# Kernel tuning notes

Measured on AMD Instinct MI355X. Metric: run time of the kernel, lower is better.

## Reference

```python
import jax, jax.numpy as jnp
import numpy as np

K_HOPS = 10
ALPHA = 0.1
N_NODES = 50000
N_EDGES = 600000
F_IN = 128
HIDDEN = 64
N_CLASSES = 40


def setup_inputs() -> dict:
    key = jax.random.key(0)
    k1, k2, k3, k4 = jax.random.split(key, 4)
    x = jax.random.normal(k1, (N_NODES, F_IN), dtype=jnp.float32)
    edge_index = jax.random.randint(k2, (2, N_EDGES), 0, N_NODES, dtype=jnp.int32)
    edge_weight = jnp.ones((N_EDGES,), dtype=jnp.float32)
    W1 = jax.random.normal(k3, (F_IN, HIDDEN), dtype=jnp.float32) * (1.0 / np.sqrt(F_IN))
    b1 = jnp.zeros((HIDDEN,), dtype=jnp.float32)
    W2 = jax.random.normal(k4, (HIDDEN, N_CLASSES), dtype=jnp.float32) * (1.0 / np.sqrt(HIDDEN))
    b2 = jnp.zeros((N_CLASSES,), dtype=jnp.float32)
    return {"x": x, "edge_index": edge_index, "edge_weight": edge_weight,
            "W1": W1, "b1": b1, "W2": W2, "b2": b2}


def reference(x, edge_index, edge_weight, W1, b1, W2, b2):
    n = x.shape[0]
    # GCN symmetric normalization with self-loops (tfg gcn cache)
    self_idx = jnp.arange(n, dtype=edge_index.dtype)
    row = jnp.concatenate([edge_index[0], self_idx])
    col = jnp.concatenate([edge_index[1], self_idx])
    w = jnp.concatenate([edge_weight, jnp.ones((n,), dtype=edge_weight.dtype)])
    deg = jax.ops.segment_sum(w, row, num_segments=n)
    dinv = jnp.where(deg > 0, jax.lax.rsqrt(jnp.maximum(deg, 1e-12)), 0.0)
    nw = dinv[row] * w * dinv[col]  # [E+N] normalized edge weights

    def prop(h):
        # h_out[i] = sum_{(i,j)} nw * h[j]
        return jax.ops.segment_sum(h[col] * nw[:, None], row, num_segments=n)

    def step(h, _):
        h_next = prop(h)
        return h_next, None

    # SSGC: out = (1-alpha)/K * sum_{l=1..K} T^l x + alpha * x
    def step_acc(carry, _):
        h, acc = carry
        h_next = prop(h)
        return (h_next, acc + h_next), None

    (_, acc), _ = jax.lax.scan(step_acc, (x, jnp.zeros_like(x)), None, length=K_HOPS)
    h = (1.0 - ALPHA) / K_HOPS * acc + ALPHA * x  # [N, F]

    h = jax.nn.relu(h @ W1 + b1)  # [N, HIDDEN]
    logits = h @ W2 + b2          # [N, N_CLASSES]
    return logits
```

## Files before the change

kernel.cpp:

```cpp
#include <hip/hip_runtime.h>
#include <hip/hip_fp16.h>
#include <math.h>

constexpr int   N   = 50000;
constexpr int   E   = 600000;
constexpr int   FIN = 128;
constexpr int   H   = 64;
constexpr int   C   = 40;
constexpr int   K   = 10;
constexpr float CK  = (1.0f - 0.1f) / 10.0f;
constexpr float AL  = 0.1f;

typedef float v2f __attribute__((ext_vector_type(2)));

__device__ __forceinline__ unsigned pack_fp8x4(float f0, float f1, float f2, float f3) {
    unsigned r = __builtin_amdgcn_cvt_pk_fp8_f32(f0, f1, 0u, false);
    r = __builtin_amdgcn_cvt_pk_fp8_f32(f2, f3, r, true);
    return r;
}

__device__ __forceinline__ float ep_w(unsigned v) {
    return __half2float(__ushort_as_half((unsigned short)(v >> 16)));
}
__device__ __forceinline__ unsigned ep_pack(int c, float w) {
    return (unsigned)(unsigned short)c |
           ((unsigned)__half_as_ushort(__float2half_rn(w)) << 16);
}

__device__ __forceinline__ void accum4(float* s, unsigned v, float w) {
    v2f p0 = __builtin_amdgcn_cvt_pk_f32_fp8(v, false);
    v2f p1 = __builtin_amdgcn_cvt_pk_f32_fp8(v, true);
    s[0] = fmaf(w, p0.x, s[0]); s[1] = fmaf(w, p0.y, s[1]);
    s[2] = fmaf(w, p1.x, s[2]); s[3] = fmaf(w, p1.y, s[3]);
}

constexpr int G1N  = 64;
constexpr int XPAD = 132;
__global__ __launch_bounds__(256, 2) void k_gemm1(const float* __restrict__ x,
                                                  const float* __restrict__ W1,
                                                  float* __restrict__ y0,
                                                  unsigned char* __restrict__ y0f8) {
    __shared__ float ws[FIN * H];
    __shared__ float xs[G1N * XPAD];
    const float4* W14 = (const float4*)W1;
    const float4* x4  = (const float4*)x;
    int t = threadIdx.x;
    int node0 = blockIdx.x * G1N;
    for (int i = t; i < FIN * H / 4; i += 256) ((float4*)ws)[i] = W14[i];
    for (int p = 0; p < 8; ++p) {
        int idx = p * 256 + t;
        int n   = idx >> 5;
        int kk  = idx & 31;
        int node = node0 + n;
        float4 v = (node < N) ? x4[(size_t)node * (FIN / 4) + kk]
                              : make_float4(0.f, 0.f, 0.f, 0.f);
        *(float4*)(xs + n * XPAD + kk * 4) = v;
    }
    __syncthreads();
    int nb = (t >> 4) * 4;
    int cb = (t & 15) * 4;
    float a00=0,a01=0,a02=0,a03=0, a10=0,a11=0,a12=0,a13=0;
    float a20=0,a21=0,a22=0,a23=0, a30=0,a31=0,a32=0,a33=0;
#pragma unroll 8
    for (int k = 0; k < FIN; ++k) {
        float4 wv = *(const float4*)(ws + k * H + cb);
        float x0 = xs[(nb + 0) * XPAD + k];
        float x1 = xs[(nb + 1) * XPAD + k];
        float x2 = xs[(nb + 2) * XPAD + k];
        float x3 = xs[(nb + 3) * XPAD + k];
        a00 = fmaf(x0, wv.x, a00); a01 = fmaf(x0, wv.y, a01);
        a02 = fmaf(x0, wv.z, a02); a03 = fmaf(x0, wv.w, a03);
        a10 = fmaf(x1, wv.x, a10); a11 = fmaf(x1, wv.y, a11);
        a12 = fmaf(x1, wv.z, a12); a13 = fmaf(x1, wv.w, a13);
        a20 = fmaf(x2, wv.x, a20); a21 = fmaf(x2, wv.y, a21);
        a22 = fmaf(x2, wv.z, a22); a23 = fmaf(x2, wv.w, a23);
        a30 = fmaf(x3, wv.x, a30); a31 = fmaf(x3, wv.y, a31);
        a32 = fmaf(x3, wv.z, a32); a33 = fmaf(x3, wv.w, a33);
    }
    float4 rows[4] = {make_float4(a00,a01,a02,a03), make_float4(a10,a11,a12,a13),
                      make_float4(a20,a21,a22,a23), make_float4(a30,a31,a32,a33)};
#pragma unroll
    for (int i = 0; i < 4; ++i) {
        int node = node0 + nb + i;
        if (node >= N) break;
        float4 r = rows[i];
        *(float4*)(y0 + (size_t)node * H + cb) = r;
        *(unsigned*)(y0f8 + (size_t)node * H + cb) = pack_fp8x4(r.x, r.y, r.z, r.w);
    }
}

__global__ __launch_bounds__(256) void k_count(const int* __restrict__ row,
                                               int* __restrict__ cnt8,
                                               unsigned short* __restrict__ rank) {
    int base = blockIdx.x * 1024 + threadIdx.x;
    int copy = blockIdx.x & 7;
#pragma unroll
    for (int i = 0; i < 4; ++i) {
        int e = base + i * 256;
        if (e < E) {
            int r = row[e];
            int old = atomicAdd(&cnt8[(size_t)copy * N + r], 1);
            rank[e] = (unsigned short)old;
        }
    }
}

__global__ __launch_bounds__(1024) void k_scan_blocks(const int* __restrict__ cnt8,
                                                      int* __restrict__ row_ptr,
                                                      int* __restrict__ bsum) {
    __shared__ int s[1024];
    int gid = blockIdx.x * 1024 + threadIdx.x;
    int v = 0;
    if (gid < N) {
#pragma unroll
        for (int c = 0; c < 8; ++c) v += cnt8[(size_t)c * N + gid];
        v = (v + 3) & ~3;
    }
    s[threadIdx.x] = v;
    __syncthreads();
    for (int off = 1; off < 1024; off <<= 1) {
        int t = (threadIdx.x >= off) ? s[threadIdx.x - off] : 0;
        __syncthreads();
        s[threadIdx.x] += t;
        __syncthreads();
    }
    if (gid < N) row_ptr[gid] = s[threadIdx.x] - v;
    if (threadIdx.x == 1023) bsum[blockIdx.x] = s[1023];
}

__global__ void k_scan_sums(const int* __restrict__ bsum, int* __restrict__ boff, int nb,
                            int* __restrict__ rowN) {
    int lane = threadIdx.x;
    int orig = (lane < nb) ? bsum[lane] : 0;
    int v = orig;
    for (int off = 1; off < 64; off <<= 1) {
        int t = __shfl_up(v, off, 64);
        if (lane >= off) v += t;
    }
    if (lane < nb) boff[lane] = v - orig;
    if (lane == nb - 1) *rowN = v;
}

__global__ __launch_bounds__(1024) void k_addoff(int* __restrict__ row_ptr,
                                                 const int* __restrict__ boff,
                                                 int* __restrict__ cnt8,
                                                 unsigned* __restrict__ ep) {
    int gid = blockIdx.x * 1024 + threadIdx.x;
    if (gid < N) {
        int rp = row_ptr[gid] + boff[blockIdx.x];
        row_ptr[gid] = rp;
        int off = rp;
        int real = 0;
#pragma unroll
        for (int c = 0; c < 8; ++c) {
            int t = cnt8[(size_t)c * N + gid];
            cnt8[(size_t)c * N + gid] = off;
            off += t;
            real += t;
        }
        int pd = (real + 3) & ~3;
        for (int j = real; j < pd; ++j) ep[rp + j] = 0u;
    }
    if (gid == 0) {
        int tot = row_ptr[N];
        *(uint4*)(ep + tot) = make_uint4(0u, 0u, 0u, 0u);
    }
}

__global__ __launch_bounds__(256) void k_scatter(const int* __restrict__ row,
                                                 const int* __restrict__ col,
                                                 const float* __restrict__ w,
                                                 const unsigned short* __restrict__ rank,
                                                 const int* __restrict__ base8,
                                                 unsigned* __restrict__ ep) {
    int base = blockIdx.x * 1024 + threadIdx.x;
    int copy = blockIdx.x & 7;
#pragma unroll
    for (int i = 0; i < 4; ++i) {
        int e = base + i * 256;
        if (e < E) {
            int r = row[e];
            int p = base8[(size_t)copy * N + r] + rank[e];
            ep[p] = ep_pack(col[e], w[e]);
        }
    }
}

__global__ void k_deg_dinv(const unsigned* __restrict__ ep, const int* __restrict__ row_ptr,
                           float* __restrict__ dinv, float* __restrict__ dinv2) {
    int i = blockIdx.x * blockDim.x + threadIdx.x;
    if (i >= N) return;
    float d = 1.0f;
    int e0 = row_ptr[i], e1 = row_ptr[i + 1];
    for (int j = e0; j < e1; ++j) d += ep_w(ep[j]);
    float di = rsqrtf(d);
    dinv[i]  = di;
    dinv2[i] = di * di;
}

__global__ __launch_bounds__(256) void k_norm(unsigned* __restrict__ ep,
                                              const int* __restrict__ row_ptr,
                                              const float* __restrict__ dinv) {
    int node = blockIdx.x * 32 + (threadIdx.x >> 3);
    if (node >= N) return;
    int l = threadIdx.x & 7;
    float dr = dinv[node];
    int e0 = row_ptr[node], e1 = row_ptr[node + 1];
    for (int j = e0 + l; j < e1; j += 8) {
        unsigned v = ep[j];
        int c = v & 0xFFFFu;
        ep[j] = ep_pack(c, ep_w(v) * dr * dinv[c]);
    }
}

constexpr int HSP = 68;
template <bool WRITE_H, bool ACC_INIT, bool FINAL>
__global__ __launch_bounds__(256) void k_prop(const unsigned* __restrict__ hin,
                                              unsigned* __restrict__ hout,
                                              __half* __restrict__ acch,
                                              const float* __restrict__ dinv2,
                                              const int* __restrict__ row_ptr,
                                              const unsigned* __restrict__ ep,
                                              const float4* __restrict__ y04,
                                              const float* __restrict__ b1,
                                              const float* __restrict__ W2,
                                              const float* __restrict__ b2,
                                              float* __restrict__ out) {
    extern __shared__ float smem[];
    float* w2s = smem;
    float* hs  = smem + H * C;
    float* b2s = hs + 16 * HSP;
    float* b1s = b2s + C;
    int t = threadIdx.x;
    if (FINAL) {
        for (int i = t; i < H * C; i += 256) w2s[i] = W2[i];
        if (t < C) b2s[t] = b2[t];
        if (t < H) b1s[t] = b1[t];
        __syncthreads();
    }
    int lane = t & 63;
    int nib  = (t >> 6) * 4 + (lane >> 4);
    int l    = lane & 15;
    int node = blockIdx.x * 16 + nib;
    bool nv  = node < N;
    int nodec = nv ? node : N - 1;
    int start = row_ptr[nodec];
    int pdeg  = nv ? (row_ptr[nodec + 1] - start) : 0;
    int md = pdeg;
#pragma unroll
    for (int off = 16; off <= 32; off <<= 1) md = max(md, __shfl_xor(md, off, 64));

    size_t base = (size_t)nodec * 16 + l;
    unsigned vself = hin[base];
    float d2       = dinv2[nodec];
    uint2* ap = (uint2*)(acch + (size_t)nodec * H + l * 4);
    uint2 old;
    if (nv && (FINAL || !ACC_INIT)) old = *ap;

    float s[4];
#pragma unroll
    for (int i = 0; i < 4; ++i) s[i] = 0.f;

    const unsigned* rp = ep + start;
    uint4 ea = *(const uint4*)rp;
    uint4 eb = *(const uint4*)(rp + ((4 < pdeg) ? 4 : 0));
    for (int batch = 0; batch < md; batch += 8) {
        uint4 ca = ea, cb = eb;
        int n0 = batch + 8, n1 = batch + 12;
        ea = *(const uint4*)(rp + ((n0 < pdeg) ? n0 : 0));
        eb = *(const uint4*)(rp + ((n1 < pdeg) ? n1 : 0));
        unsigned v0 = hin[(size_t)(ca.x & 0xFFFFu) * 16 + l];
        unsigned v1 = hin[(size_t)(ca.y & 0xFFFFu) * 16 + l];
        unsigned v2 = hin[(size_t)(ca.z & 0xFFFFu) * 16 + l];
        unsigned v3 = hin[(size_t)(ca.w & 0xFFFFu) * 16 + l];
        unsigned v4 = hin[(size_t)(cb.x & 0xFFFFu) * 16 + l];
        unsigned v5 = hin[(size_t)(cb.y & 0xFFFFu) * 16 + l];
        unsigned v6 = hin[(size_t)(cb.z & 0xFFFFu) * 16 + l];
        unsigned v7 = hin[(size_t)(cb.w & 0xFFFFu) * 16 + l];
        accum4(s, v0, (batch     < pdeg) ? ep_w(ca.x) : 0.0f);
        accum4(s, v1, (batch + 1 < pdeg) ? ep_w(ca.y) : 0.0f);
        accum4(s, v2, (batch + 2 < pdeg) ? ep_w(ca.z) : 0.0f);
        accum4(s, v3, (batch + 3 < pdeg) ? ep_w(ca.w) : 0.0f);
        accum4(s, v4, (batch + 4 < pdeg) ? ep_w(cb.x) : 0.0f);
        accum4(s, v5, (batch + 5 < pdeg) ? ep_w(cb.y) : 0.0f);
        accum4(s, v6, (batch + 6 < pdeg) ? ep_w(cb.z) : 0.0f);
        accum4(s, v7, (batch + 7 < pdeg) ? ep_w(cb.w) : 0.0f);
    }
    if (nv) {
        accum4(s, vself, d2);
        if (WRITE_H) {
            hout[base] = pack_fp8x4(s[0], s[1], s[2], s[3]);
        }
        if (FINAL) {
            const unsigned* u = (const unsigned*)&old;
#pragma unroll
            for (int d = 0; d < 2; ++d) {
                float2 f = __half22float2(*(__half2*)&u[d]);
                s[2*d+0] += f.x; s[2*d+1] += f.y;
            }
            float4 ya = y04[(size_t)nodec * (H / 4) + l];
            const float* bp = b1s + l * 4;
            float* hp = hs + nib * HSP + l * 4;
            hp[0] = fmaxf(fmaf(CK, s[0], fmaf(AL, ya.x, bp[0])), 0.f);
            hp[1] = fmaxf(fmaf(CK, s[1], fmaf(AL, ya.y, bp[1])), 0.f);
            hp[2] = fmaxf(fmaf(CK, s[2], fmaf(AL, ya.z, bp[2])), 0.f);
            hp[3] = fmaxf(fmaf(CK, s[3], fmaf(AL, ya.w, bp[3])), 0.f);
        } else {
            if (!ACC_INIT) {
                const unsigned* u = (const unsigned*)&old;
#pragma unroll
                for (int d = 0; d < 2; ++d) {
                    float2 f = __half22float2(*(__half2*)&u[d]);
                    s[2*d+0] += f.x; s[2*d+1] += f.y;
                }
            }
            uint2 nvp;
            unsigned* u = (unsigned*)&nvp;
#pragma unroll
            for (int d = 0; d < 2; ++d) {
                __half2 h = __floats2half2_rn(s[2*d+0], s[2*d+1]);
                u[d] = *(unsigned*)&h;
            }
            *ap = nvp;
        }
    }
    if (FINAL) {
        __syncthreads();
        int node0 = blockIdx.x * 16;
        for (int o = t; o < 16 * C; o += 256) {
            int nl = o / C, c = o % C;
            int n2 = node0 + nl;
            if (n2 >= N) continue;
            float v = b2s[c];
            const float* hr = &hs[nl * HSP];
#pragma unroll
            for (int k = 0; k < H; ++k) v = fmaf(hr[k], w2s[k * C + c], v);
            out[n2 * C + c] = v;
        }
    }
}

extern "C" void kernel_launch(void* const* d_in, const int* in_sizes, int n_in,
                              void* d_out, int out_size, void* d_ws, size_t ws_size,
                              hipStream_t stream) {
    const float* x  = (const float*)d_in[0];
    const int*   ei = (const int*)d_in[1];
    const float* ew = (const float*)d_in[2];
    const float* W1 = (const float*)d_in[3];
    const float* b1 = (const float*)d_in[4];
    const float* W2 = (const float*)d_in[5];
    const float* b2 = (const float*)d_in[6];
    float* out = (float*)d_out;

    const int* row = ei;
    const int* col = ei + E;

    char* ws = (char*)d_ws;
    size_t off = 0;
    auto alloc = [&](size_t bytes) -> char* {
        char* p = ws + off;
        off = (off + bytes + 1023) & ~(size_t)1023;
        return p;
    };
    constexpr size_t EPAD = (size_t)E + 3 * (size_t)N + 1024;
    float*          y0   = (float*)alloc((size_t)N * H * 4);
    unsigned char*  y0f8 = (unsigned char*)alloc((size_t)N * H);
    unsigned char*  ha   = (unsigned char*)alloc((size_t)N * H);
    unsigned char*  hb   = (unsigned char*)alloc((size_t)N * H);
    __half*         acch = (__half*)alloc((size_t)N * H * 2);
    int*            cnt8 = (int*)alloc((size_t)8 * N * 4);
    unsigned short* rank = (unsigned short*)alloc((size_t)E * 2);
    float*    dinv   = (float*)   alloc((size_t)N * 4);
    float*    dinv2  = (float*)   alloc((size_t)N * 4);
    int*      row_ptr= (int*)     alloc((size_t)(N + 1) * 4);
    int*      bsum   = (int*)     alloc(64 * 4);
    int*      boff   = (int*)     alloc(64 * 4);
    unsigned* ep     = (unsigned*)alloc(EPAD * 4);

    hipMemsetAsync(cnt8, 0, (size_t)8 * N * 4, stream);

    k_gemm1<<<(N + G1N - 1) / G1N, 256, 0, stream>>>(x, W1, y0, y0f8);

    k_count<<<(E + 1023) / 1024, 256, 0, stream>>>(row, cnt8, rank);

    constexpr int NB = (N + 1023) / 1024;
    k_scan_blocks<<<NB, 1024, 0, stream>>>(cnt8, row_ptr, bsum);
    k_scan_sums<<<1, 64, 0, stream>>>(bsum, boff, NB, row_ptr + N);
    k_addoff<<<NB, 1024, 0, stream>>>(row_ptr, boff, cnt8, ep);

    k_scatter<<<(E + 1023) / 1024, 256, 0, stream>>>(row, col, ew, rank, cnt8, ep);
    k_deg_dinv<<<(N + 255) / 256, 256, 0, stream>>>(ep, row_ptr, dinv, dinv2);
    k_norm<<<(N + 31) / 32, 256, 0, stream>>>(ep, row_ptr, dinv);

    const unsigned* hin = (const unsigned*)y0f8;
    unsigned* bufs[2] = {(unsigned*)ha, (unsigned*)hb};
    const float4* y04 = (const float4*)y0;
    int grid = (N + 15) / 16;
    size_t smemF = (size_t)(H * C + 16 * HSP + C + H) * 4;
    for (int hop = 0; hop < K; ++hop) {
        unsigned* hout = bufs[hop & 1];
        if (hop == 0)
            k_prop<true, true, false><<<grid, 256, 0, stream>>>(hin, hout, acch, dinv2,
                row_ptr, ep, y04, b1, W2, b2, out);
        else if (hop == K - 1)
            k_prop<false, false, true><<<grid, 256, smemF, stream>>>(hin, hout, acch, dinv2,
                row_ptr, ep, y04, b1, W2, b2, out);
        else
            k_prop<true, false, false><<<grid, 256, 0, stream>>>(hin, hout, acch, dinv2,
                row_ptr, ep, y04, b1, W2, b2, out);
        hin = hout;
    }
}
```

Baseline: 293.1 us.

## Deepen gather prefetch in propagation and spread count kernel over more blocks

The propagation loop now software-pipelines two stages ahead: edge records are prefetched 16 entries ahead and the feature gathers for the next batch are issued before the current batch is accumulated, so more memory loads are in flight per thread. The accumulator read is moved after the neighbour loop to shorten register live ranges. The count kernel now processes one edge per thread with four times more blocks, and the scatter kernel derives the counter copy from the edge index so the two kernels stay consistent. This costs more registers in the hot kernel, which may lower occupancy.

```diff
diff --git a/kernel.cpp b/kernel.cpp
--- a/kernel.cpp
+++ b/kernel.cpp
@@ -92,17 +92,12 @@
 __global__ __launch_bounds__(256) void k_count(const int* __restrict__ row,
                                                int* __restrict__ cnt8,
                                                unsigned short* __restrict__ rank) {
-    int base = blockIdx.x * 1024 + threadIdx.x;
+    int e = blockIdx.x * 256 + threadIdx.x;
+    if (e >= E) return;
     int copy = blockIdx.x & 7;
-#pragma unroll
-    for (int i = 0; i < 4; ++i) {
-        int e = base + i * 256;
-        if (e < E) {
-            int r = row[e];
-            int old = atomicAdd(&cnt8[(size_t)copy * N + r], 1);
-            rank[e] = (unsigned short)old;
-        }
-    }
+    int r = row[e];
+    int old = atomicAdd(&cnt8[(size_t)copy * N + r], 1);
+    rank[e] = (unsigned short)old;
 }
 
 __global__ __launch_bounds__(1024) void k_scan_blocks(const int* __restrict__ cnt8,
@@ -174,11 +169,11 @@
                                                  const int* __restrict__ base8,
                                                  unsigned* __restrict__ ep) {
     int base = blockIdx.x * 1024 + threadIdx.x;
-    int copy = blockIdx.x & 7;
 #pragma unroll
     for (int i = 0; i < 4; ++i) {
         int e = base + i * 256;
         if (e < E) {
+            int copy = (e >> 8) & 7;
             int r = row[e];
             int p = base8[(size_t)copy * N + r] + rank[e];
             ep[p] = ep_pack(col[e], w[e]);
@@ -253,45 +248,58 @@
     size_t base = (size_t)nodec * 16 + l;
     unsigned vself = hin[base];
     float d2       = dinv2[nodec];
-    uint2* ap = (uint2*)(acch + (size_t)nodec * H + l * 4);
-    uint2 old;
-    if (nv && (FINAL || !ACC_INIT)) old = *ap;
 
     float s[4];
 #pragma unroll
     for (int i = 0; i < 4; ++i) s[i] = 0.f;
 
     const unsigned* rp = ep + start;
-    uint4 ea = *(const uint4*)rp;
-    uint4 eb = *(const uint4*)(rp + ((4 < pdeg) ? 4 : 0));
-    for (int batch = 0; batch < md; batch += 8) {
-        uint4 ca = ea, cb = eb;
-        int n0 = batch + 8, n1 = batch + 12;
-        ea = *(const uint4*)(rp + ((n0 < pdeg) ? n0 : 0));
-        eb = *(const uint4*)(rp + ((n1 < pdeg) ? n1 : 0));
-        unsigned v0 = hin[(size_t)(ca.x & 0xFFFFu) * 16 + l];
-        unsigned v1 = hin[(size_t)(ca.y & 0xFFFFu) * 16 + l];
-        unsigned v2 = hin[(size_t)(ca.z & 0xFFFFu) * 16 + l];
-        unsigned v3 = hin[(size_t)(ca.w & 0xFFFFu) * 16 + l];
-        unsigned v4 = hin[(size_t)(cb.x & 0xFFFFu) * 16 + l];
-        unsigned v5 = hin[(size_t)(cb.y & 0xFFFFu) * 16 + l];
-        unsigned v6 = hin[(size_t)(cb.z & 0xFFFFu) * 16 + l];
-        unsigned v7 = hin[(size_t)(cb.w & 0xFFFFu) * 16 + l];
-        accum4(s, v0, (batch     < pdeg) ? ep_w(ca.x) : 0.0f);
-        accum4(s, v1, (batch + 1 < pdeg) ? ep_w(ca.y) : 0.0f);
-        accum4(s, v2, (batch + 2 < pdeg) ? ep_w(ca.z) : 0.0f);
-        accum4(s, v3, (batch + 3 < pdeg) ? ep_w(ca.w) : 0.0f);
-        accum4(s, v4, (batch + 4 < pdeg) ? ep_w(cb.x) : 0.0f);
-        accum4(s, v5, (batch + 5 < pdeg) ? ep_w(cb.y) : 0.0f);
-        accum4(s, v6, (batch + 6 < pdeg) ? ep_w(cb.z) : 0.0f);
-        accum4(s, v7, (batch + 7 < pdeg) ? ep_w(cb.w) : 0.0f);
+    if (md > 0) {
+        uint4 rA0 = *(const uint4*)rp;
+        uint4 rA1 = *(const uint4*)(rp + ((4  < pdeg) ? 4  : 0));
+        uint4 rB0 = *(const uint4*)(rp + ((8  < pdeg) ? 8  : 0));
+        uint4 rB1 = *(const uint4*)(rp + ((12 < pdeg) ? 12 : 0));
+        unsigned g0 = hin[(size_t)(rA0.x & 0xFFFFu) * 16 + l];
+        unsigned g1 = hin[(size_t)(rA0.y & 0xFFFFu) * 16 + l];
+        unsigned g2 = hin[(size_t)(rA0.z & 0xFFFFu) * 16 + l];
+        unsigned g3 = hin[(size_t)(rA0.w & 0xFFFFu) * 16 + l];
+        unsigned g4 = hin[(size_t)(rA1.x & 0xFFFFu) * 16 + l];
+        unsigned g5 = hin[(size_t)(rA1.y & 0xFFFFu) * 16 + l];
+        unsigned g6 = hin[(size_t)(rA1.z & 0xFFFFu) * 16 + l];
+        unsigned g7 = hin[(size_t)(rA1.w & 0xFFFFu) * 16 + l];
+        for (int b = 0; b < md; b += 8) {
+            int n0 = b + 16, n1 = b + 20;
+            uint4 rC0 = *(const uint4*)(rp + ((n0 < pdeg) ? n0 : 0));
+            uint4 rC1 = *(const uint4*)(rp + ((n1 < pdeg) ? n1 : 0));
+            unsigned h0 = hin[(size_t)(rB0.x & 0xFFFFu) * 16 + l];
+            unsigned h1 = hin[(size_t)(rB0.y & 0xFFFFu) * 16 + l];
+            unsigned h2 = hin[(size_t)(rB0.z & 0xFFFFu) * 16 + l];
+            unsigned h3 = hin[(size_t)(rB0.w & 0xFFFFu) * 16 + l];
+            unsigned h4 = hin[(size_t)(rB1.x & 0xFFFFu) * 16 + l];
+            unsigned h5 = hin[(size_t)(rB1.y & 0xFFFFu) * 16 + l];
+            unsigned h6 = hin[(size_t)(rB1.z & 0xFFFFu) * 16 + l];
+            unsigned h7 = hin[(size_t)(rB1.w & 0xFFFFu) * 16 + l];
+            accum4(s, g0, (b     < pdeg) ? ep_w(rA0.x) : 0.0f);
+            accum4(s, g1, (b + 1 < pdeg) ? ep_w(rA0.y) : 0.0f);
+            accum4(s, g2, (b + 2 < pdeg) ? ep_w(rA0.z) : 0.0f);
+            accum4(s, g3, (b + 3 < pdeg) ? ep_w(rA0.w) : 0.0f);
+            accum4(s, g4, (b + 4 < pdeg) ? ep_w(rA1.x) : 0.0f);
+            accum4(s, g5, (b + 5 < pdeg) ? ep_w(rA1.y) : 0.0f);
+            accum4(s, g6, (b + 6 < pdeg) ? ep_w(rA1.z) : 0.0f);
+            accum4(s, g7, (b + 7 < pdeg) ? ep_w(rA1.w) : 0.0f);
+            rA0 = rB0; rA1 = rB1; rB0 = rC0; rB1 = rC1;
+            g0 = h0; g1 = h1; g2 = h2; g3 = h3;
+            g4 = h4; g5 = h5; g6 = h6; g7 = h7;
+        }
     }
     if (nv) {
         accum4(s, vself, d2);
         if (WRITE_H) {
             hout[base] = pack_fp8x4(s[0], s[1], s[2], s[3]);
         }
+        uint2* ap = (uint2*)(acch + (size_t)nodec * H + l * 4);
         if (FINAL) {
+            uint2 old = *ap;
             const unsigned* u = (const unsigned*)&old;
 #pragma unroll
             for (int d = 0; d < 2; ++d) {
@@ -307,6 +315,7 @@
             hp[3] = fmaxf(fmaf(CK, s[3], fmaf(AL, ya.w, bp[3])), 0.f);
         } else {
             if (!ACC_INIT) {
+                uint2 old = *ap;
                 const unsigned* u = (const unsigned*)&old;
 #pragma unroll
                 for (int d = 0; d < 2; ++d) {
@@ -381,7 +390,7 @@
 
     k_gemm1<<<(N + G1N - 1) / G1N, 256, 0, stream>>>(x, W1, y0, y0f8);
 
-    k_count<<<(E + 1023) / 1024, 256, 0, stream>>>(row, cnt8, rank);
+    k_count<<<(E + 255) / 256, 256, 0, stream>>>(row, cnt8, rank);
 
     constexpr int NB = (N + 1023) / 1024;
     k_scan_blocks<<<NB, 1024, 0, stream>>>(cnt8, row_ptr, bsum);
```

Measured after the change: 294.0 us. About the same (+0.3%).

## Select count-copy by XCC id and fuse block-sum scan into offset kernel

Applied to the files above, without the earlier changes.

The edge-count kernel now picks its atomic counter copy from the hardware XCC id rather than the block index, so atomics from each XCD hit that XCD's own copy. The copy index is packed into the high bits of the per-edge rank so the scatter kernel can recover it. The single-wave block-sum scan kernel is folded into the offset kernel, which removes one launch. This relies on per-row ranks staying below 8192 and on the XCC_ID register encoding being correct for this GPU.

```diff
diff --git a/kernel.cpp b/kernel.cpp
--- a/kernel.cpp
+++ b/kernel.cpp
@@ -12,6 +12,8 @@
 constexpr float AL  = 0.1f;
 
 typedef float v2f __attribute__((ext_vector_type(2)));
+
+#define XCC_ID_SIMM ((31 << 11) | 20)
 
 __device__ __forceinline__ unsigned pack_fp8x4(float f0, float f1, float f2, float f3) {
     unsigned r = __builtin_amdgcn_cvt_pk_fp8_f32(f0, f1, 0u, false);
@@ -92,17 +94,12 @@
 __global__ __launch_bounds__(256) void k_count(const int* __restrict__ row,
                                                int* __restrict__ cnt8,
                                                unsigned short* __restrict__ rank) {
-    int base = blockIdx.x * 1024 + threadIdx.x;
-    int copy = blockIdx.x & 7;
-#pragma unroll
-    for (int i = 0; i < 4; ++i) {
-        int e = base + i * 256;
-        if (e < E) {
-            int r = row[e];
-            int old = atomicAdd(&cnt8[(size_t)copy * N + r], 1);
-            rank[e] = (unsigned short)old;
-        }
-    }
+    int e = blockIdx.x * 256 + threadIdx.x;
+    if (e >= E) return;
+    unsigned copy = __builtin_amdgcn_s_getreg(XCC_ID_SIMM) & 7u;
+    int r = row[e];
+    int old = atomicAdd(&cnt8[(size_t)copy * N + r], 1);
+    rank[e] = (unsigned short)(old | (copy << 13));
 }
 
 __global__ __launch_bounds__(1024) void k_scan_blocks(const int* __restrict__ cnt8,
@@ -128,26 +125,28 @@
     if (threadIdx.x == 1023) bsum[blockIdx.x] = s[1023];
 }
 
-__global__ void k_scan_sums(const int* __restrict__ bsum, int* __restrict__ boff, int nb,
-                            int* __restrict__ rowN) {
-    int lane = threadIdx.x;
-    int orig = (lane < nb) ? bsum[lane] : 0;
-    int v = orig;
-    for (int off = 1; off < 64; off <<= 1) {
-        int t = __shfl_up(v, off, 64);
-        if (lane >= off) v += t;
-    }
-    if (lane < nb) boff[lane] = v - orig;
-    if (lane == nb - 1) *rowN = v;
-}
-
+constexpr int NB = (N + 1023) / 1024;
 __global__ __launch_bounds__(1024) void k_addoff(int* __restrict__ row_ptr,
-                                                 const int* __restrict__ boff,
+                                                 const int* __restrict__ bsum,
                                                  int* __restrict__ cnt8,
                                                  unsigned* __restrict__ ep) {
+    __shared__ int sboff;
+    __shared__ int stot;
+    if (threadIdx.x < 64) {
+        int lane = threadIdx.x;
+        int orig = (lane < NB) ? bsum[lane] : 0;
+        int v = orig;
+        for (int off = 1; off < 64; off <<= 1) {
+            int t = __shfl_up(v, off, 64);
+            if (lane >= off) v += t;
+        }
+        if (lane == (int)blockIdx.x) sboff = v - orig;
+        if (lane == NB - 1)          stot  = v;
+    }
+    __syncthreads();
     int gid = blockIdx.x * 1024 + threadIdx.x;
     if (gid < N) {
-        int rp = row_ptr[gid] + boff[blockIdx.x];
+        int rp = row_ptr[gid] + sboff;
         row_ptr[gid] = rp;
         int off = rp;
         int real = 0;
@@ -162,8 +161,8 @@
         for (int j = real; j < pd; ++j) ep[rp + j] = 0u;
     }
     if (gid == 0) {
-        int tot = row_ptr[N];
-        *(uint4*)(ep + tot) = make_uint4(0u, 0u, 0u, 0u);
+        row_ptr[N] = stot;
+        *(uint4*)(ep + stot) = make_uint4(0u, 0u, 0u, 0u);
     }
 }
 
@@ -174,13 +173,14 @@
                                                  const int* __restrict__ base8,
                                                  unsigned* __restrict__ ep) {
     int base = blockIdx.x * 1024 + threadIdx.x;
-    int copy = blockIdx.x & 7;
 #pragma unroll
     for (int i = 0; i < 4; ++i) {
         int e = base + i * 256;
         if (e < E) {
+            unsigned rk = rank[e];
+            int copy = rk >> 13;
             int r = row[e];
-            int p = base8[(size_t)copy * N + r] + rank[e];
+            int p = base8[(size_t)copy * N + r] + (rk & 0x1FFF);
             ep[p] = ep_pack(col[e], w[e]);
         }
     }
@@ -374,19 +374,16 @@
     float*    dinv2  = (float*)   alloc((size_t)N * 4);
     int*      row_ptr= (int*)     alloc((size_t)(N + 1) * 4);
     int*      bsum   = (int*)     alloc(64 * 4);
-    int*      boff   = (int*)     alloc(64 * 4);
     unsigned* ep     = (unsigned*)alloc(EPAD * 4);
 
     hipMemsetAsync(cnt8, 0, (size_t)8 * N * 4, stream);
 
     k_gemm1<<<(N + G1N - 1) / G1N, 256, 0, stream>>>(x, W1, y0, y0f8);
 
-    k_count<<<(E + 1023) / 1024, 256, 0, stream>>>(row, cnt8, rank);
-
-    constexpr int NB = (N + 1023) / 1024;
+    k_count<<<(E + 255) / 256, 256, 0, stream>>>(row, cnt8, rank);
+
     k_scan_blocks<<<NB, 1024, 0, stream>>>(cnt8, row_ptr, bsum);
-    k_scan_sums<<<1, 64, 0, stream>>>(bsum, boff, NB, row_ptr + N);
-    k_addoff<<<NB, 1024, 0, stream>>>(row_ptr, boff, cnt8, ep);
+    k_addoff<<<NB, 1024, 0, stream>>>(row_ptr, bsum, cnt8, ep);
 
     k_scatter<<<(E + 1023) / 1024, 256, 0, stream>>>(row, col, ew, rank, cnt8, ep);
     k_deg_dinv<<<(N + 255) / 256, 256, 0, stream>>>(ep, row_ptr, dinv, dinv2);
```

Result: no change. 291.8 us (-0.4%).
